# Kernel optimization log

Hardware: AMD Instinct MI355X
Metric: run time of the kernel (lower is better)

## Reference

```python
import jax, jax.numpy as jnp
import numpy as np

B, T, D = 16, 4096, 1024


def setup_inputs() -> dict:
    key = jax.random.key(0)
    kx, kl = jax.random.split(key)
    x = jax.random.normal(kx, (B, T, D), dtype=jnp.float32)
    seq_lens = jax.random.randint(kl, (B,), 0, T + 1, dtype=jnp.int64)
    return {"x": x, "seq_lens": seq_lens}


def reference(x, seq_lens):
    # mask[i, :length] = True over [B, T] (broadcast over D), then flatten + compact.
    # Torch's flatten()[mask.flatten()] is row-major, so within each valid (b, t)
    # the D features stay contiguous -> gather whole rows of x.reshape(B*T, D).
    b, t, d = x.shape
    valid = jnp.arange(t)[None, :] < seq_lens[:, None]          # [B, T] bool
    total_rows = int(np.asarray(seq_lens).sum())                # static under eager eval
    rows = jnp.nonzero(valid.ravel(), size=total_rows, fill_value=0)[0]  # [total_rows]
    return x.reshape(b * t, d)[rows].reshape(-1)                # [total_rows * D]
```

## Files before the change

### kernel.cpp

```cpp
#include <hip/hip_runtime.h>


#define DD 1024
#define TT 4096

__global__ void prefix_kernel(const void* __restrict__ seq_raw, int n,
                              int total_rows, int* __restrict__ prefix) {
    if (blockIdx.x == 0 && threadIdx.x == 0) {
        const int*       s32 = (const int*)seq_raw;
        const long long* s64 = (const long long*)seq_raw;
        long long sum32 = 0;
        for (int i = 0; i < n; ++i) sum32 += (long long)s32[i];
        const bool use32 = (sum32 == (long long)total_rows);
        int acc = 0;
        for (int i = 0; i < n; ++i) {
            prefix[i] = acc;
            acc += use32 ? s32[i] : (int)s64[i];
        }
        prefix[n] = acc;
    }
}

__global__ __launch_bounds__(256) void gather_rows(
        const float* __restrict__ x, const int* __restrict__ prefix,
        float* __restrict__ out, int n_b) {
    const int r = blockIdx.x;
    int b = 0;
    for (int i = 1; i <= n_b; ++i) b += (prefix[i] <= r) ? 1 : 0;
    const int t = r - prefix[b];
    const float4* __restrict__ src =
        (const float4*)(x + ((size_t)b * TT + (size_t)t) * DD);
    float4* __restrict__ dst = (float4*)(out + (size_t)r * DD);
    dst[threadIdx.x] = src[threadIdx.x];
}

extern "C" void kernel_launch(void* const* d_in, const int* in_sizes, int n_in,
                              void* d_out, int out_size, void* d_ws, size_t ws_size,
                              hipStream_t stream) {
    const float* x   = (const float*)d_in[0];
    const void*  seq = d_in[1];
    const int    n_b = in_sizes[1];
    float*       out = (float*)d_out;
    int*      prefix = (int*)d_ws;

    const int total_rows = out_size / DD;

    prefix_kernel<<<1, 64, 0, stream>>>(seq, n_b, total_rows, prefix);
    if (total_rows > 0) {
        gather_rows<<<total_rows, 256, 0, stream>>>(x, prefix, out, n_b);
    }
}
```

Baseline: 344.5 us.

## Fuse prefix computation into persistent gather kernel with 8-row batching

```diff
diff --git a/kernel.cpp b/kernel.cpp
--- a/kernel.cpp
+++ b/kernel.cpp
@@ -3,35 +3,103 @@
 
 #define DD 1024
 #define TT 4096
+#define F4 256
+#define NB 16
 
-__global__ void prefix_kernel(const void* __restrict__ seq_raw, int n,
-                              int total_rows, int* __restrict__ prefix) {
-    if (blockIdx.x == 0 && threadIdx.x == 0) {
+typedef float f4 __attribute__((ext_vector_type(4)));
+
+__global__ __launch_bounds__(256) void gather16(
+        const float* __restrict__ x, const void* __restrict__ seq_raw,
+        float* __restrict__ out, int total_rows) {
+    const int tid = threadIdx.x;
+
+    const int*       s32 = (const int*)seq_raw;
+    const long long* s64 = (const long long*)seq_raw;
+    long long sum32 = 0;
+#pragma unroll
+    for (int i = 0; i < NB; ++i) sum32 += (long long)s32[i];
+    const bool use32 = (sum32 == (long long)total_rows);
+
+    int preA[NB];
+    int cA[NB];
+    int acc = 0;
+    if (use32) {
+#pragma unroll
+        for (int i = 0; i < NB; ++i) {
+            preA[i] = acc; cA[i] = i * TT - acc; acc += s32[i];
+        }
+    } else {
+#pragma unroll
+        for (int i = 0; i < NB; ++i) {
+            preA[i] = acc; cA[i] = i * TT - acc; acc += (int)s64[i];
+        }
+    }
+
+    const f4* __restrict__ x4 = (const f4*)x;
+    f4* __restrict__ o4       = (f4*)out;
+
+    const int nG = (total_rows + 7) >> 3;
+    for (int g = blockIdx.x; g < nG; g += gridDim.x) {
+        const int r0 = g << 3;
+        if (r0 + 8 <= total_rows) {
+            f4 v[8];
+#pragma unroll
+            for (int k = 0; k < 8; ++k) {
+                const int rr = r0 + k;
+                int corr = 0;
+#pragma unroll
+                for (int i = 1; i < NB; ++i)
+                    corr = (preA[i] <= rr) ? cA[i] : corr;
+                v[k] = __builtin_nontemporal_load(
+                           &x4[(size_t)(rr + corr) * F4 + tid]);
+            }
+#pragma unroll
+            for (int k = 0; k < 8; ++k)
+                __builtin_nontemporal_store(
+                    v[k], &o4[(size_t)(r0 + k) * F4 + tid]);
+        } else {
+            for (int k = 0; k < 8; ++k) {
+                const int rr = r0 + k;
+                if (rr >= total_rows) break;
+                int corr = 0;
+#pragma unroll
+                for (int i = 1; i < NB; ++i)
+                    corr = (preA[i] <= rr) ? cA[i] : corr;
+                o4[(size_t)rr * F4 + tid] = x4[(size_t)(rr + corr) * F4 + tid];
+            }
+        }
+    }
+}
+
+__global__ __launch_bounds__(256) void gather_generic(
+        const float* __restrict__ x, const void* __restrict__ seq_raw,
+        float* __restrict__ out, int n_b, int total_rows) {
+    __shared__ int pre_s[1025];
+    if (threadIdx.x == 0) {
         const int*       s32 = (const int*)seq_raw;
         const long long* s64 = (const long long*)seq_raw;
         long long sum32 = 0;
-        for (int i = 0; i < n; ++i) sum32 += (long long)s32[i];
+        for (int i = 0; i < n_b; ++i) sum32 += (long long)s32[i];
         const bool use32 = (sum32 == (long long)total_rows);
         int acc = 0;
-        for (int i = 0; i < n; ++i) {
-            prefix[i] = acc;
-            acc += use32 ? s32[i] : (int)s64[i];
+        if (use32) {
+            for (int i = 0; i < n_b; ++i) { pre_s[i] = acc; acc += s32[i]; }
+        } else {
+            for (int i = 0; i < n_b; ++i) { pre_s[i] = acc; acc += (int)s64[i]; }
         }
-        prefix[n] = acc;
+        pre_s[n_b] = acc;
     }
-}
+    __syncthreads();
 
-__global__ __launch_bounds__(256) void gather_rows(
-        const float* __restrict__ x, const int* __restrict__ prefix,
-        float* __restrict__ out, int n_b) {
-    const int r = blockIdx.x;
-    int b = 0;
-    for (int i = 1; i <= n_b; ++i) b += (prefix[i] <= r) ? 1 : 0;
-    const int t = r - prefix[b];
-    const float4* __restrict__ src =
-        (const float4*)(x + ((size_t)b * TT + (size_t)t) * DD);
-    float4* __restrict__ dst = (float4*)(out + (size_t)r * DD);
-    dst[threadIdx.x] = src[threadIdx.x];
+    const f4* __restrict__ x4 = (const f4*)x;
+    f4* __restrict__ o4       = (f4*)out;
+    for (int r = blockIdx.x; r < total_rows; r += gridDim.x) {
+        int b = 0;
+        for (int i = 1; i < n_b; ++i) b += (pre_s[i] <= r) ? 1 : 0;
+        const int t = r - pre_s[b];
+        o4[(size_t)r * F4 + threadIdx.x] =
+            x4[((size_t)b * TT + t) * F4 + threadIdx.x];
+    }
 }
 
 extern "C" void kernel_launch(void* const* d_in, const int* in_sizes, int n_in,
@@ -41,12 +109,16 @@
     const void*  seq = d_in[1];
     const int    n_b = in_sizes[1];
     float*       out = (float*)d_out;
-    int*      prefix = (int*)d_ws;
 
     const int total_rows = out_size / DD;
+    if (total_rows <= 0) return;
 
-    prefix_kernel<<<1, 64, 0, stream>>>(seq, n_b, total_rows, prefix);
-    if (total_rows > 0) {
-        gather_rows<<<total_rows, 256, 0, stream>>>(x, prefix, out, n_b);
+    if (n_b == NB) {
+        const int nG = (total_rows + 7) >> 3;
+        const int grid = nG < 2048 ? nG : 2048;
+        gather16<<<grid, 256, 0, stream>>>(x, seq, out, total_rows);
+    } else {
+        const int grid = total_rows < 2048 ? total_rows : 2048;
+        gather_generic<<<grid, 256, 0, stream>>>(x, seq, out, n_b, total_rows);
     }
 }
```

Measured after the change: 342.4 us. No clear change (-0.6%).
